# Performance work log

Hardware: AMD Instinct MI355X
Metric: run time of the kernel (lower is better)

Reference implementation:

```python
import jax, jax.numpy as jnp
import numpy as np

# Bit index 0 = LSB of the IEEE-754 uint32 pattern (little-endian bit order):
# bits[..., 0:23] mantissa, bits[..., 23:31] exponent, bits[..., 31] sign.
_SHIFTS = jnp.arange(32, dtype=jnp.uint32)


def f32_to_bits(x):
    """float32 [...] -> pulse bits [..., 32] in {0., 1.}."""
    u = jax.lax.bitcast_convert_type(x, jnp.uint32)
    return ((u[..., None] >> _SHIFTS) & jnp.uint32(1)).astype(jnp.float32)


def bits_to_f32(b):
    """pulse bits [..., 32] -> float32 [...]. Exact inverse of f32_to_bits."""
    u = jnp.sum(b.astype(jnp.uint32) << _SHIFTS, axis=-1, dtype=jnp.uint32)
    return jax.lax.bitcast_convert_type(u, jnp.float32)


def setup_inputs() -> dict:
    key = jax.random.key(0)
    kA, kB = jax.random.split(key)
    # Encode realistic fp32 values into pulse (bit) tensors.
    A_vals = jax.random.normal(kA, (4, 512, 512), dtype=jnp.float32)   # [B, M, K]
    B_vals = jax.random.normal(kB, (512, 512), dtype=jnp.float32)      # [K, N]
    return {"A": f32_to_bits(A_vals), "B": f32_to_bits(B_vals)}


def reference(A, B):
    """Spike-domain FP32 matmul: decode pulses -> fp32 GEMM -> re-encode pulses.

    A: [..., M, K, 32] pulses, B: [K, N, 32] pulses -> C: [..., M, N, 32] pulses.
    The spiking multiplier/adder gates implement exact IEEE-754 fp32 multiply
    and sequential accumulation over k, i.e. C[..., i, j] = sum_k A[...,i,k]*B[k,j]
    in fp32.
    """
    A_f = bits_to_f32(A)                         # [B, M, K]
    B_f = bits_to_f32(B)                         # [K, N]
    C = jnp.einsum('bmk,kn->bmn', A_f, B_f)      # fp32 accumulation
    return f32_to_bits(C)                        # [B, M, N, 32]
```

## Files before the change

### kernel.cpp

```cpp
#include <hip/hip_runtime.h>
#include <stdint.h>

#define BATCH 4
#define MDIM  512
#define KDIM  512
#define NDIM  512
#define ROWS  (BATCH * MDIM)
#define BR    4
#define BCOLS 256

__device__ __forceinline__ uint32_t spread4(uint32_t x) {
    x = (x | (x << 12)) & 0x000F000Fu;
    x = (x | (x << 6))  & 0x03030303u;
    x = (x | (x << 3))  & 0x11111111u;
    return x;
}

__global__ __launch_bounds__(256) void decode_all(const float* __restrict__ Abits,
                                                  const float* __restrict__ Bbits,
                                                  uint32_t* __restrict__ Au,
                                                  uint32_t* __restrict__ Bu,
                                                  int wordsA, int wordsB) {
    const int lane = threadIdx.x & 63;
    const int waveId = (blockIdx.x * blockDim.x + threadIdx.x) >> 6;
    const int totalWaves = (gridDim.x * blockDim.x) >> 6;
    const int totalWords = wordsA + wordsB;
    const int sh = lane & 56;

    for (int wb = waveId * 8; wb < totalWords; wb += totalWaves * 8) {
        const float* src;
        uint32_t* dst;
        if (wb < wordsA) { src = Abits + (size_t)wb * 32;            dst = Au + wb; }
        else             { src = Bbits + (size_t)(wb - wordsA) * 32; dst = Bu + (wb - wordsA); }

        uint4 v = ((const uint4*)src)[lane];
        unsigned long long m0 = __ballot((v.x >> 29) & 1u);
        unsigned long long m1 = __ballot((v.y >> 29) & 1u);
        unsigned long long m2 = __ballot((v.z >> 29) & 1u);
        unsigned long long m3 = __ballot((v.w >> 29) & 1u);

        if ((lane & 7) == 0) {
            uint32_t w = (spread4((uint32_t)(m0 >> sh) & 0xFFu) << 0)
                       | (spread4((uint32_t)(m1 >> sh) & 0xFFu) << 1)
                       | (spread4((uint32_t)(m2 >> sh) & 0xFFu) << 2)
                       | (spread4((uint32_t)(m3 >> sh) & 0xFFu) << 3);
            dst[lane >> 3] = w;
        }
    }
}

__global__ __launch_bounds__(256) void gemm_encode(const float* __restrict__ A,
                                                   const float* __restrict__ B,
                                                   float* __restrict__ outbits) {
    __shared__ uint32_t Us[BR][BCOLS];

    const int tid = threadIdx.x;
    const int rowBase = blockIdx.x * BR;
    const int n0 = blockIdx.y * BCOLS;
    const int n = n0 + tid;

    float acc[BR];
#pragma unroll
    for (int r = 0; r < BR; ++r) acc[r] = 0.0f;

    const float* Bcol = B + n;
    const float* Arow = A + (size_t)rowBase * KDIM;

    for (int k0 = 0; k0 < KDIM; k0 += 4) {
        float b0 = Bcol[(size_t)(k0 + 0) * NDIM];
        float b1 = Bcol[(size_t)(k0 + 1) * NDIM];
        float b2 = Bcol[(size_t)(k0 + 2) * NDIM];
        float b3 = Bcol[(size_t)(k0 + 3) * NDIM];
        float4 a[BR];
#pragma unroll
        for (int r = 0; r < BR; ++r)
            a[r] = *(const float4*)(Arow + (size_t)r * KDIM + k0);
#pragma unroll
        for (int r = 0; r < BR; ++r) {
            acc[r] = __builtin_fmaf(a[r].x, b0, acc[r]);
            acc[r] = __builtin_fmaf(a[r].y, b1, acc[r]);
            acc[r] = __builtin_fmaf(a[r].z, b2, acc[r]);
            acc[r] = __builtin_fmaf(a[r].w, b3, acc[r]);
        }
    }

#pragma unroll
    for (int r = 0; r < BR; ++r) Us[r][tid] = __float_as_uint(acc[r]);
    __syncthreads();

    float* oBase = outbits + ((size_t)rowBase * NDIM + n0) * 32;
    const int b = (tid & 7) * 4;
#pragma unroll
    for (int r = 0; r < BR; ++r) {
        float* o = oBase + (size_t)r * NDIM * 32;
#pragma unroll
        for (int it = 0; it < 8; ++it) {
            uint32_t u = Us[r][it * 32 + (tid >> 3)];
            float4 q;
            q.x = (float)((u >> (b + 0)) & 1u);
            q.y = (float)((u >> (b + 1)) & 1u);
            q.z = (float)((u >> (b + 2)) & 1u);
            q.w = (float)((u >> (b + 3)) & 1u);
            *(float4*)(o + it * 1024 + tid * 4) = q;
        }
    }
}

extern "C" void kernel_launch(void* const* d_in, const int* in_sizes, int n_in,
                              void* d_out, int out_size, void* d_ws, size_t ws_size,
                              hipStream_t stream) {
    const float* Abits = (const float*)d_in[0];
    const float* Bbits = (const float*)d_in[1];
    float* out = (float*)d_out;

    const int nA = in_sizes[0];
    const int nB = in_sizes[1];
    const int wordsA = nA >> 5;
    const int wordsB = nB >> 5;

    uint32_t* A_u = (uint32_t*)d_ws;
    uint32_t* B_u = A_u + wordsA;

    decode_all<<<2048, 256, 0, stream>>>(Abits, Bbits, A_u, B_u, wordsA, wordsB);

    dim3 grid(ROWS / BR, NDIM / BCOLS);
    gemm_encode<<<grid, 256, 0, stream>>>((const float*)A_u, (const float*)B_u, out);
}
```

Measured before the change: 87.20 us.

## Unroll decode to two loads per wave, double GEMM row tile, unroll k loop

The decode kernel now uses compile-time sizes and a fully unrolled loop in which each wave handles 16 words, issuing two 1KB loads before its ballots so more memory requests are in flight. The GEMM row block grows from 4 to 8 rows, so each B load is reused across more rows, and the k loop is unrolled by 4. The larger row tile halves the GEMM grid and raises register use, which can lower occupancy on a kernel that already launches few blocks.

```diff
diff --git a/kernel.cpp b/kernel.cpp
--- a/kernel.cpp
+++ b/kernel.cpp
@@ -6,8 +6,15 @@
 #define KDIM  512
 #define NDIM  512
 #define ROWS  (BATCH * MDIM)
-#define BR    4
+#define BR    8
 #define BCOLS 256
+
+#define WORDS_A (ROWS * KDIM)
+#define WORDS_B (KDIM * NDIM)
+#define WORDS_T (WORDS_A + WORDS_B)
+#define DEC_BLOCKS 2048
+#define DEC_WAVES  (DEC_BLOCKS * 4)
+#define DEC_ITERS  (WORDS_T / (16 * DEC_WAVES))
 
 __device__ __forceinline__ uint32_t spread4(uint32_t x) {
     x = (x | (x << 12)) & 0x000F000Fu;
@@ -19,32 +26,42 @@
 __global__ __launch_bounds__(256) void decode_all(const float* __restrict__ Abits,
                                                   const float* __restrict__ Bbits,
                                                   uint32_t* __restrict__ Au,
-                                                  uint32_t* __restrict__ Bu,
-                                                  int wordsA, int wordsB) {
+                                                  uint32_t* __restrict__ Bu) {
     const int lane = threadIdx.x & 63;
     const int waveId = (blockIdx.x * blockDim.x + threadIdx.x) >> 6;
-    const int totalWaves = (gridDim.x * blockDim.x) >> 6;
-    const int totalWords = wordsA + wordsB;
     const int sh = lane & 56;
 
-    for (int wb = waveId * 8; wb < totalWords; wb += totalWaves * 8) {
+#pragma unroll
+    for (int i = 0; i < DEC_ITERS; ++i) {
+        const int wb = (waveId + i * DEC_WAVES) * 16;
         const float* src;
         uint32_t* dst;
-        if (wb < wordsA) { src = Abits + (size_t)wb * 32;            dst = Au + wb; }
-        else             { src = Bbits + (size_t)(wb - wordsA) * 32; dst = Bu + (wb - wordsA); }
+        if (wb < WORDS_A) { src = Abits + (size_t)wb * 32;           dst = Au + wb; }
+        else              { src = Bbits + (size_t)(wb - WORDS_A) * 32; dst = Bu + (wb - WORDS_A); }
 
-        uint4 v = ((const uint4*)src)[lane];
-        unsigned long long m0 = __ballot((v.x >> 29) & 1u);
-        unsigned long long m1 = __ballot((v.y >> 29) & 1u);
-        unsigned long long m2 = __ballot((v.z >> 29) & 1u);
-        unsigned long long m3 = __ballot((v.w >> 29) & 1u);
+        uint4 v0 = ((const uint4*)src)[lane];
+        uint4 v1 = ((const uint4*)src)[lane + 64];
+
+        unsigned long long a0 = __ballot((v0.x >> 29) & 1u);
+        unsigned long long a1 = __ballot((v0.y >> 29) & 1u);
+        unsigned long long a2 = __ballot((v0.z >> 29) & 1u);
+        unsigned long long a3 = __ballot((v0.w >> 29) & 1u);
+        unsigned long long b0 = __ballot((v1.x >> 29) & 1u);
+        unsigned long long b1 = __ballot((v1.y >> 29) & 1u);
+        unsigned long long b2 = __ballot((v1.z >> 29) & 1u);
+        unsigned long long b3 = __ballot((v1.w >> 29) & 1u);
 
         if ((lane & 7) == 0) {
-            uint32_t w = (spread4((uint32_t)(m0 >> sh) & 0xFFu) << 0)
-                       | (spread4((uint32_t)(m1 >> sh) & 0xFFu) << 1)
-                       | (spread4((uint32_t)(m2 >> sh) & 0xFFu) << 2)
-                       | (spread4((uint32_t)(m3 >> sh) & 0xFFu) << 3);
-            dst[lane >> 3] = w;
+            uint32_t w0 = (spread4((uint32_t)(a0 >> sh) & 0xFFu) << 0)
+                        | (spread4((uint32_t)(a1 >> sh) & 0xFFu) << 1)
+                        | (spread4((uint32_t)(a2 >> sh) & 0xFFu) << 2)
+                        | (spread4((uint32_t)(a3 >> sh) & 0xFFu) << 3);
+            uint32_t w1 = (spread4((uint32_t)(b0 >> sh) & 0xFFu) << 0)
+                        | (spread4((uint32_t)(b1 >> sh) & 0xFFu) << 1)
+                        | (spread4((uint32_t)(b2 >> sh) & 0xFFu) << 2)
+                        | (spread4((uint32_t)(b3 >> sh) & 0xFFu) << 3);
+            dst[lane >> 3] = w0;
+            dst[8 + (lane >> 3)] = w1;
         }
     }
 }
@@ -66,6 +83,7 @@
     const float* Bcol = B + n;
     const float* Arow = A + (size_t)rowBase * KDIM;
 
+#pragma unroll 4
     for (int k0 = 0; k0 < KDIM; k0 += 4) {
         float b0 = Bcol[(size_t)(k0 + 0) * NDIM];
         float b1 = Bcol[(size_t)(k0 + 1) * NDIM];
@@ -113,15 +131,10 @@
     const float* Bbits = (const float*)d_in[1];
     float* out = (float*)d_out;
 
-    const int nA = in_sizes[0];
-    const int nB = in_sizes[1];
-    const int wordsA = nA >> 5;
-    const int wordsB = nB >> 5;
+    uint32_t* A_u = (uint32_t*)d_ws;
+    uint32_t* B_u = A_u + WORDS_A;
 
-    uint32_t* A_u = (uint32_t*)d_ws;
-    uint32_t* B_u = A_u + wordsA;
-
-    decode_all<<<2048, 256, 0, stream>>>(Abits, Bbits, A_u, B_u, wordsA, wordsB);
+    decode_all<<<DEC_BLOCKS, 256, 0, stream>>>(Abits, Bbits, A_u, B_u);
 
     dim3 grid(ROWS / BR, NDIM / BCOLS);
     gemm_encode<<<grid, 256, 0, stream>>>((const float*)A_u, (const float*)B_u, out);
```

Result: slower. 124.1 us (+42.3%).
